# Kernel optimization log

Measured on AMD Instinct MI355X. Metric: run time of the kernel, lower is better.

The kernel has to match this reference:

```python
import jax, jax.numpy as jnp
import numpy as np

TEMP1, TEMP2, TEMP3 = 4.0, 5.0, 10.0  # forward() default temps
EPS = 1e-8


def setup_inputs() -> dict:
    key = jax.random.key(0)
    k1, k2 = jax.random.split(key)
    B, L, D = 64, 64, 512
    return {
        "ecg_embs": jax.random.normal(k1, (B, L, D), dtype=jnp.float32),
        "sent_embs": jax.random.normal(k2, (B, L, D), dtype=jnp.float32),
    }


def reference(ecg_embs, sent_embs):
    # Fully-batched version of the original per-sample Python loop.
    # i indexes the sentence (query) sample, j the ecg (context) sample.
    B, L, D = ecg_embs.shape
    # scores[i,j,s,q] = <ecg[j,s,:], sent[i,q,:]>  == contextT @ query in torch
    scores = jnp.einsum('jsd,iqd->ijsq', ecg_embs, sent_embs)
    # 1st softmax over query axis q
    attn = jax.nn.softmax(scores, axis=-1)
    # transpose to (i,j,q,s), temperature-scale, 2nd softmax over source axis s
    attn = jax.nn.softmax(TEMP1 * jnp.swapaxes(attn, -1, -2), axis=-1)  # (i,j,q,s)
    # weightedContext[i,j,q,:] = sum_s attn[i,j,q,s] * ecg[j,s,:]
    wctx = jnp.einsum('ijqs,jsd->ijqd', attn, ecg_embs)
    sent = sent_embs[:, None]  # (i,1,q,d) broadcast over j
    w12 = jnp.sum(sent * wctx, axis=-1)
    w1 = jnp.linalg.norm(sent, axis=-1)
    w2 = jnp.linalg.norm(wctx, axis=-1)
    cos = w12 / jnp.maximum(w1 * w2, EPS)  # (i,j,q)
    # row_sim.mul_(temp2).exp_().sum(dim=1).log() ; similarities[j,i] (cat along dim=1)
    sim = TEMP3 * jnp.log(jnp.sum(jnp.exp(TEMP2 * cos), axis=-1)).T  # (j,i)
    labels = jnp.arange(B)
    logp0 = jax.nn.log_softmax(sim, axis=-1)
    logp1 = jax.nn.log_softmax(sim.T, axis=-1)
    loss0 = -jnp.mean(logp0[labels, labels])
    loss1 = -jnp.mean(logp1[labels, labels])
    # att_maps: list of attn[i] from iteration i == diagonal (i==j) attention,
    # each shaped (1, queryL, ih=1, iw=sourceL); stacked -> (B, 1, L, 1, L)
    att_maps = attn[labels, labels][:, None, :, None, :]
    return (loss0 + loss1) / 2.0, att_maps
```

## Files before the change

kernel.cpp:

```cpp
#include <hip/hip_runtime.h>
#include <math.h>

typedef __attribute__((ext_vector_type(8))) short short8;
typedef __attribute__((ext_vector_type(4))) float f32x4;
typedef unsigned int uint;
typedef unsigned short ushort;

#define T1 4.0f
#define T2 5.0f
#define T3 10.0f
#define EPSF 1e-8f
#define SST 68

__device__ inline ushort f2bf(float x) {
    union { float f; uint u; } a; a.f = x;
    uint r = a.u + 0x7FFFu + ((a.u >> 16) & 1u);
    return (ushort)(r >> 16);
}
__device__ inline float bf2f(ushort h) {
    union { uint u; float f; } a; a.u = ((uint)h) << 16;
    return a.f;
}

#define GLDS(gsrc, ldst) \
    __builtin_amdgcn_global_load_lds( \
        (const __attribute__((address_space(1))) uint*)(gsrc), \
        (__attribute__((address_space(3))) uint*)(ldst), 16, 0, 0)

__global__ __launch_bounds__(256) void prep_kernel(
        const float* __restrict__ ecg, const float* __restrict__ sent,
        char* __restrict__ EH, char* __restrict__ EL,
        char* __restrict__ SH, char* __restrict__ SL, float* __restrict__ w1) {
    __shared__ float rs[32][2];
    const int bid = blockIdx.x;
    const int tensor = bid >> 7, idx = (bid >> 1) & 63, half = bid & 1;
    const float* src = (tensor ? sent : ecg) + (size_t)idx * 32768;
    char* dh = (tensor ? SH : EH) + (size_t)idx * 65536;
    char* dl = (tensor ? SL : EL) + (size_t)idx * 65536;
    const int tid = threadIdx.x;
    const int w = tid >> 6, l = tid & 63;

    if (tid < 64) { rs[tid >> 1][tid & 1] = 0.f; }
    __syncthreads();

    const int kc   = 8 * (w & 1) + (l >> 3);
    const int c    = (l >> 1) & 3;
    const int col  = 256 * (w & 1) + l * 4;
    const int wsel = w & 1;

    #pragma unroll
    for (int g = 0; g < 16; g++) {
        int r = 32 * half + 2 * g + (w >> 1);
        float4 v = *(const float4*)(src + (size_t)r * 512 + col);
        ushort h0 = f2bf(v.x), h1 = f2bf(v.y), h2 = f2bf(v.z), h3 = f2bf(v.w);
        uint2 H; H.x = (uint)h0 | ((uint)h1 << 16); H.y = (uint)h2 | ((uint)h3 << 16);
        ushort l0 = f2bf(v.x - bf2f(h0)), l1 = f2bf(v.y - bf2f(h1));
        ushort l2 = f2bf(v.z - bf2f(h2)), l3 = f2bf(v.w - bf2f(h3));
        uint2 L; L.x = (uint)l0 | ((uint)l1 << 16); L.y = (uint)l2 | ((uint)l3 << 16);
        size_t off = (size_t)kc * 4096 + r * 64 + ((c + (r >> 1)) & 3) * 16 + (l & 1) * 8;
        *(uint2*)(dh + off) = H;
        *(uint2*)(dl + off) = L;
        if (tensor) {
            float p = v.x * v.x + v.y * v.y + v.z * v.z + v.w * v.w;
            #pragma unroll
            for (int o = 32; o; o >>= 1) p += __shfl_xor(p, o);
            if (l == 0) rs[2 * g + (w >> 1)][wsel] += p;
        }
    }
    __syncthreads();
    if (tensor && tid < 32)
        w1[idx * 64 + 32 * half + tid] = sqrtf(rs[tid][0] + rs[tid][1]);
}

__global__ __launch_bounds__(256) void gprep_kernel(
        const char* __restrict__ EH, const char* __restrict__ EL, char* __restrict__ Gp) {
    __shared__ __align__(16) char lds[8192];
    const int j = blockIdx.x;
    const int tid = threadIdx.x;
    const int wv = tid >> 6, lane = tid & 63;
    const int wq = wv >> 1, wn = wv & 1;
    const int quad = lane >> 4, ln = lane & 15;
    const char* srcH = EH + (size_t)j * 65536 + wv * 1024 + lane * 16;
    const char* srcL = EL + (size_t)j * 65536 + wv * 1024 + lane * 16;

    int ao[2], bo[2];
    #pragma unroll
    for (int mi = 0; mi < 2; mi++) {
        int R = 32 * wq + 16 * mi + ln;
        ao[mi] = R * 64 + ((quad + (R >> 1)) & 3) * 16;
    }
    #pragma unroll
    for (int ni = 0; ni < 2; ni++) {
        int R = 32 * wn + 16 * ni + ln;
        bo[ni] = R * 64 + ((quad + (R >> 1)) & 3) * 16;
    }

    f32x4 acc[2][2];
    #pragma unroll
    for (int a = 0; a < 2; a++)
        #pragma unroll
        for (int b = 0; b < 2; b++) acc[a][b] = (f32x4){0.f, 0.f, 0.f, 0.f};

    for (int kc = 0; kc < 16; kc++) {
        GLDS(srcH + (size_t)kc * 4096, lds + wv * 1024);
        GLDS(srcL + (size_t)kc * 4096, lds + 4096 + wv * 1024);
        __syncthreads();
        short8 ah[2], al[2], bh[2], bl[2];
        #pragma unroll
        for (int mi = 0; mi < 2; mi++) {
            ah[mi] = *(const short8*)(lds + ao[mi]);
            al[mi] = *(const short8*)(lds + 4096 + ao[mi]);
        }
        #pragma unroll
        for (int ni = 0; ni < 2; ni++) {
            bh[ni] = *(const short8*)(lds + bo[ni]);
            bl[ni] = *(const short8*)(lds + 4096 + bo[ni]);
        }
        #pragma unroll
        for (int mi = 0; mi < 2; mi++)
            #pragma unroll
            for (int ni = 0; ni < 2; ni++) {
                acc[mi][ni] = __builtin_amdgcn_mfma_f32_16x16x32_bf16(ah[mi], bh[ni], acc[mi][ni], 0, 0, 0);
                acc[mi][ni] = __builtin_amdgcn_mfma_f32_16x16x32_bf16(ah[mi], bl[ni], acc[mi][ni], 0, 0, 0);
                acc[mi][ni] = __builtin_amdgcn_mfma_f32_16x16x32_bf16(al[mi], bh[ni], acc[mi][ni], 0, 0, 0);
            }
        __syncthreads();
    }
    #pragma unroll
    for (int mi = 0; mi < 2; mi++)
        #pragma unroll
        for (int ni = 0; ni < 2; ni++)
            #pragma unroll
            for (int r = 0; r < 4; r++) {
                int t = 32 * wq + 16 * mi + quad * 4 + r;
                int u = 32 * wn + 16 * ni + ln;
                float g = acc[mi][ni][r];
                ushort h = f2bf(g);
                ushort l = f2bf(g - bf2f(h));
                char* base = Gp + (size_t)j * 16384 + t * 128 + (((u >> 3) + t) & 7) * 16 + (u & 7) * 2;
                *(ushort*)base = h;
                *(ushort*)(base + 8192) = l;
            }
}

__global__ __launch_bounds__(256, 4) void pair_kernel(
        const char* __restrict__ EH, const char* __restrict__ EL,
        const char* __restrict__ SH, const char* __restrict__ SL,
        const char* __restrict__ Gp, const float* __restrict__ w1g,
        float* __restrict__ simval, float* __restrict__ out) {

    __shared__ __align__(16) char lds[33792];
    __shared__ __align__(16) float mz[64];
    __shared__ float w12all[256], w2all[256];
    __shared__ float mpart[64][2], spart[64][2];

    const int tid = threadIdx.x;
    const int bn = blockIdx.x;
    const int xcd = bn & 7, slot = bn >> 3;
    const int T = xcd * 8 + (slot >> 4);
    const int wp = slot & 15;
    const int bi = (T >> 3) * 4 + (wp >> 2);
    const int bj = (T & 7) * 4 + (wp & 3);
    const int i0 = bi * 2, j0 = bj * 2;

    const int wv = tid >> 6, lane = tid & 63;
    const int wq = wv >> 1, wn = wv & 1;
    const int quad = lane >> 4, ln = lane & 15;

    int aoff[4], boff[4];
    #pragma unroll
    for (int mi = 0; mi < 4; mi++) {
        int R = 64 * (mi >> 1) + 32 * wq + 16 * (mi & 1) + ln;
        aoff[mi] = R * 64 + ((quad + (R >> 1)) & 3) * 16;
    }
    #pragma unroll
    for (int ni = 0; ni < 4; ni++) {
        int R = 64 * (ni >> 1) + 32 * wn + 16 * (ni & 1) + ln;
        boff[ni] = 16384 + R * 64 + ((quad + (R >> 1)) & 3) * 16;
    }

    const char* gA; const char* gB; int ldoff;
    if (wv == 0)      { gA = EH + (size_t)j0 * 65536;       gB = EH + (size_t)(j0 + 1) * 65536; ldoff = 0; }
    else if (wv == 1) { gA = EL + (size_t)j0 * 65536;       gB = EL + (size_t)(j0 + 1) * 65536; ldoff = 8192; }
    else if (wv == 2) { gA = SH + (size_t)i0 * 65536;       gB = SH + (size_t)(i0 + 1) * 65536; ldoff = 16384; }
    else              { gA = SL + (size_t)i0 * 65536;       gB = SL + (size_t)(i0 + 1) * 65536; ldoff = 24576; }
    gA += lane * 16; gB += lane * 16;

    f32x4 acc[4][4];
    #pragma unroll
    for (int a = 0; a < 4; a++)
        #pragma unroll
        for (int b = 0; b < 4; b++) acc[a][b] = (f32x4){0.f, 0.f, 0.f, 0.f};

    for (int kc = 0; kc < 16; kc++) {
        #pragma unroll
        for (int n = 0; n < 4; n++) GLDS(gA + n * 1024, lds + ldoff + n * 1024);
        #pragma unroll
        for (int n = 0; n < 4; n++) GLDS(gB + n * 1024, lds + ldoff + 4096 + n * 1024);
        gA += 4096; gB += 4096;
        __syncthreads();
        short8 bh[4], bl[4];
        #pragma unroll
        for (int ni = 0; ni < 4; ni++) {
            bh[ni] = *(const short8*)(lds + boff[ni]);
            bl[ni] = *(const short8*)(lds + boff[ni] + 8192);
        }
        #pragma unroll
        for (int mi = 0; mi < 4; mi++) {
            short8 ah = *(const short8*)(lds + aoff[mi]);
            short8 al = *(const short8*)(lds + aoff[mi] + 8192);
            #pragma unroll
            for (int ni = 0; ni < 4; ni++) {
                acc[mi][ni] = __builtin_amdgcn_mfma_f32_16x16x32_bf16(ah, bh[ni], acc[mi][ni], 0, 0, 0);
                acc[mi][ni] = __builtin_amdgcn_mfma_f32_16x16x32_bf16(ah, bl[ni], acc[mi][ni], 0, 0, 0);
                acc[mi][ni] = __builtin_amdgcn_mfma_f32_16x16x32_bf16(al, bh[ni], acc[mi][ni], 0, 0, 0);
            }
        }
        __syncthreads();
    }

    float* SsT = (float*)lds;
    float* yT  = (float*)lds;
    char*  Pb  = lds + 17408;

    #pragma unroll
    for (int pr = 0; pr < 4; pr++) {
        const int a = pr >> 1, b = pr & 1;
        const int i = i0 + b, j = j0 + a;

        #pragma unroll
        for (int dm = 0; dm < 2; dm++)
            #pragma unroll
            for (int dn = 0; dn < 2; dn++) {
                int s0 = 32 * wq + 16 * dm + quad * 4;
                int q  = 32 * wn + 16 * dn + ln;
                *(f32x4*)(SsT + q * SST + s0) = acc[2 * a + dm][2 * b + dn];
            }
        #pragma unroll
        for (int dm = 0; dm < 2; dm++)
            #pragma unroll
            for (int r = 0; r < 4; r++) {
                float v0 = acc[2 * a + dm][2 * b + 0][r];
                float v1 = acc[2 * a + dm][2 * b + 1][r];
                float m = fmaxf(v0, v1);
                m = fmaxf(m, __shfl_xor(m, 1));
                m = fmaxf(m, __shfl_xor(m, 2));
                m = fmaxf(m, __shfl_xor(m, 4));
                m = fmaxf(m, __shfl_xor(m, 8));
                float e = __expf(v0 - m) + __expf(v1 - m);
                e += __shfl_xor(e, 1);
                e += __shfl_xor(e, 2);
                e += __shfl_xor(e, 4);
                e += __shfl_xor(e, 8);
                if (ln == 0) {
                    int s = 32 * wq + 16 * dm + quad * 4 + r;
                    mpart[s][wn] = m;
                    spart[s][wn] = e;
                }
            }
        __syncthreads();

        if (tid < 64) {
            float m0 = mpart[tid][0], m1 = mpart[tid][1];
            float mm = fmaxf(m0, m1);
            float z = spart[tid][0] * __expf(m0 - mm) + spart[tid][1] * __expf(m1 - mm);
            mz[tid] = mm + __logf(z);
        }
        __syncthreads();

        {
            const int q = tid >> 2, c = tid & 3;
            float sc[16], at[16];
            #pragma unroll
            for (int r4 = 0; r4 < 4; r4++)
                *(f32x4*)(sc + 4 * r4) = *(const f32x4*)(SsT + q * SST + 16 * c + 4 * r4);
            float mzv[16];
            #pragma unroll
            for (int r4 = 0; r4 < 4; r4++)
                *(f32x4*)(mzv + 4 * r4) = *(const f32x4*)(mz + 16 * c + 4 * r4);
            float m2 = -1e30f;
            #pragma unroll
            for (int t = 0; t < 16; t++) {
                at[t] = __expf(sc[t] - mzv[t]);
                m2 = fmaxf(m2, T1 * at[t]);
            }
            m2 = fmaxf(m2, __shfl_xor(m2, 1));
            m2 = fmaxf(m2, __shfl_xor(m2, 2));
            float sum = 0.f;
            #pragma unroll
            for (int t = 0; t < 16; t++) { at[t] = __expf(T1 * at[t] - m2); sum += at[t]; }
            sum += __shfl_xor(sum, 1);
            sum += __shfl_xor(sum, 2);
            float inv = 1.f / sum;
            float p12 = 0.f;
            #pragma unroll
            for (int t = 0; t < 16; t++) { at[t] *= inv; p12 += at[t] * sc[t]; }
            p12 += __shfl_xor(p12, 1);
            p12 += __shfl_xor(p12, 2);
            if (c == 0) w12all[pr * 64 + q] = p12;

            if (i == j) {
                float* om = out + 1 + (size_t)i * 4096;
                #pragma unroll
                for (int t = 0; t < 16; t++) om[q * 64 + c * 16 + t] = at[t];
            }

            uint hw[8], lw[8];
            #pragma unroll
            for (int e = 0; e < 8; e++) {
                ushort h0 = f2bf(at[2 * e]), h1 = f2bf(at[2 * e + 1]);
                hw[e] = (uint)h0 | ((uint)h1 << 16);
                ushort l0 = f2bf(at[2 * e] - bf2f(h0)), l1 = f2bf(at[2 * e + 1] - bf2f(h1));
                lw[e] = (uint)l0 | ((uint)l1 << 16);
            }
            int p0 = (2 * c + q) & 7, p1 = (2 * c + 1 + q) & 7;
            uint4 W;
            W.x = hw[0]; W.y = hw[1]; W.z = hw[2]; W.w = hw[3];
            *(uint4*)(Pb + q * 128 + p0 * 16) = W;
            W.x = hw[4]; W.y = hw[5]; W.z = hw[6]; W.w = hw[7];
            *(uint4*)(Pb + q * 128 + p1 * 16) = W;
            W.x = lw[0]; W.y = lw[1]; W.z = lw[2]; W.w = lw[3];
            *(uint4*)(Pb + 8192 + q * 128 + p0 * 16) = W;
            W.x = lw[4]; W.y = lw[5]; W.z = lw[6]; W.w = lw[7];
            *(uint4*)(Pb + 8192 + q * 128 + p1 * 16) = W;
        }
        __syncthreads();

        {
            const char* gs = Gp + (size_t)j * 16384 + wv * 4096 + lane * 16;
            #pragma unroll
            for (int k = 0; k < 4; k++)
                GLDS(gs + k * 1024, lds + wv * 4096 + k * 1024);
        }
        __syncthreads();

        f32x4 acc2[2][2];
        #pragma unroll
        for (int x = 0; x < 2; x++)
            #pragma unroll
            for (int y = 0; y < 2; y++) acc2[x][y] = (f32x4){0.f, 0.f, 0.f, 0.f};
        #pragma unroll
        for (int ch = 0; ch < 2; ch++) {
            short8 pah[2], pal[2], gbh[2], gbl[2];
            #pragma unroll
            for (int m2i = 0; m2i < 2; m2i++) {
                int q = 32 * wq + 16 * m2i + ln;
                int ph = ((ch * 4 + quad) + q) & 7;
                pah[m2i] = *(const short8*)(Pb + q * 128 + ph * 16);
                pal[m2i] = *(const short8*)(Pb + 8192 + q * 128 + ph * 16);
            }
            #pragma unroll
            for (int n2i = 0; n2i < 2; n2i++) {
                int u = 32 * wn + 16 * n2i + ln;
                int ph = ((ch * 4 + quad) + u) & 7;
                gbh[n2i] = *(const short8*)(lds + u * 128 + ph * 16);
                gbl[n2i] = *(const short8*)(lds + 8192 + u * 128 + ph * 16);
            }
            #pragma unroll
            for (int m2i = 0; m2i < 2; m2i++)
                #pragma unroll
                for (int n2i = 0; n2i < 2; n2i++) {
                    acc2[m2i][n2i] = __builtin_amdgcn_mfma_f32_16x16x32_bf16(pah[m2i], gbh[n2i], acc2[m2i][n2i], 0, 0, 0);
                    acc2[m2i][n2i] = __builtin_amdgcn_mfma_f32_16x16x32_bf16(pah[m2i], gbl[n2i], acc2[m2i][n2i], 0, 0, 0);
                    acc2[m2i][n2i] = __builtin_amdgcn_mfma_f32_16x16x32_bf16(pal[m2i], gbh[n2i], acc2[m2i][n2i], 0, 0, 0);
                }
        }
        __syncthreads();

        #pragma unroll
        for (int m2i = 0; m2i < 2; m2i++)
            #pragma unroll
            for (int n2i = 0; n2i < 2; n2i++) {
                int q0 = 32 * wq + 16 * m2i + quad * 4;
                int t  = 32 * wn + 16 * n2i + ln;
                *(f32x4*)(yT + t * SST + q0) = acc2[m2i][n2i];
            }
        __syncthreads();

        {
            const int q = tid >> 2, c = tid & 3;
            int p0 = (2 * c + q) & 7, p1 = (2 * c + 1 + q) & 7;
            uint4 H0 = *(const uint4*)(Pb + q * 128 + p0 * 16);
            uint4 H1 = *(const uint4*)(Pb + q * 128 + p1 * 16);
            uint4 L0 = *(const uint4*)(Pb + 8192 + q * 128 + p0 * 16);
            uint4 L1 = *(const uint4*)(Pb + 8192 + q * 128 + p1 * 16);
            uint hw[8] = {H0.x,H0.y,H0.z,H0.w, H1.x,H1.y,H1.z,H1.w};
            uint lw[8] = {L0.x,L0.y,L0.z,L0.w, L1.x,L1.y,L1.z,L1.w};
            float s = 0.f;
            #pragma unroll
            for (int e = 0; e < 8; e++) {
                float q0v = bf2f((ushort)(hw[e] & 0xFFFFu)) + bf2f((ushort)(lw[e] & 0xFFFFu));
                float q1v = bf2f((ushort)(hw[e] >> 16))     + bf2f((ushort)(lw[e] >> 16));
                s += q0v * yT[(16 * c + 2 * e) * SST + q];
                s += q1v * yT[(16 * c + 2 * e + 1) * SST + q];
            }
            s += __shfl_xor(s, 1);
            s += __shfl_xor(s, 2);
            if (c == 0) w2all[pr * 64 + q] = s;
        }
        __syncthreads();
    }

    {
        const int pr = wv;
        const int ii = i0 + (pr & 1), jj = j0 + (pr >> 1);
        float w2 = sqrtf(fmaxf(w2all[pr * 64 + lane], 0.f));
        float cosv = w12all[pr * 64 + lane] / fmaxf(w1g[ii * 64 + lane] * w2, EPSF);
        float e = __expf(T2 * cosv);
        #pragma unroll
        for (int off = 32; off; off >>= 1) e += __shfl_down(e, off);
        if (lane == 0) simval[ii * 64 + jj] = T3 * __logf(e);
    }
}

__global__ __launch_bounds__(256) void loss_kernel(const float* __restrict__ val,
                                                   float* __restrict__ out) {
    __shared__ float v[4096];
    const int tid = threadIdx.x;
    #pragma unroll
    for (int k = 0; k < 4; k++)
        ((float4*)v)[tid + k * 256] = ((const float4*)val)[tid + k * 256];
    __syncthreads();
    if (tid < 64) {
        int i = tid;
        float rmax = -1e30f, cmax = -1e30f;
        for (int jj = 0; jj < 64; jj++) {
            rmax = fmaxf(rmax, v[i * 64 + jj]);
            cmax = fmaxf(cmax, v[jj * 64 + i]);
        }
        float rs = 0.f, cs = 0.f;
        for (int jj = 0; jj < 64; jj++) {
            rs += __expf(v[i * 64 + jj] - rmax);
            cs += __expf(v[jj * 64 + i] - cmax);
        }
        float rlse = rmax + __logf(rs);
        float clse = cmax + __logf(cs);
        float part = 2.f * v[i * 64 + i] - rlse - clse;
        #pragma unroll
        for (int off = 32; off; off >>= 1) part += __shfl_down(part, off);
        if (i == 0) out[0] = -part / 128.f;
    }
}

extern "C" void kernel_launch(void* const* d_in, const int* in_sizes, int n_in,
                              void* d_out, int out_size, void* d_ws, size_t ws_size,
                              hipStream_t stream) {
    (void)in_sizes; (void)n_in; (void)out_size; (void)ws_size;
    const float* ecg  = (const float*)d_in[0];
    const float* sent = (const float*)d_in[1];
    float* out = (float*)d_out;

    char* ws = (char*)d_ws;
    float* w1v  = (float*)ws;
    float* simv = (float*)(ws + 16384);
    char* EH = ws + 32768;
    char* EL = EH + (size_t)64 * 65536;
    char* SH = EL + (size_t)64 * 65536;
    char* SL = SH + (size_t)64 * 65536;
    char* Gp = SL + (size_t)64 * 65536;

    prep_kernel <<<256, 256, 0, stream>>>(ecg, sent, EH, EL, SH, SL, w1v);
    gprep_kernel<<<64,  256, 0, stream>>>(EH, EL, Gp);
    pair_kernel <<<1024, 256, 0, stream>>>(EH, EL, SH, SL, Gp, w1v, simv, out);
    loss_kernel <<<1,   256, 0, stream>>>(simv, out);
}
```

Baseline: 161.7 us.

## Drop low-bf16 attention term and restructure pair-kernel epilogue around registers

The attention matrix P is now stored only as a single bf16 high part, so the second GEMM uses two MFMAs per tile instead of three. The w2 norm is computed directly from the accumulator registers with a small partial-sum buffer, removing the yT transpose through LDS and two barriers. The first softmax now reads a swizzled, unpadded score tile from LDS, replacing the shuffle-based partial max/sum pass. The G tile is copied through registers instead of global_load_lds. The precision of P against the fp32 reference drops, which may affect tolerance.

```diff
diff --git a/kernel.cpp b/kernel.cpp
--- a/kernel.cpp
+++ b/kernel.cpp
@@ -10,7 +10,6 @@
 #define T2 5.0f
 #define T3 10.0f
 #define EPSF 1e-8f
-#define SST 68
 
 __device__ inline ushort f2bf(float x) {
     union { float f; uint u; } a; a.f = x;
@@ -149,10 +148,10 @@
         const char* __restrict__ Gp, const float* __restrict__ w1g,
         float* __restrict__ simval, float* __restrict__ out) {
 
-    __shared__ __align__(16) char lds[33792];
+    __shared__ __align__(16) char lds[32768];
     __shared__ __align__(16) float mz[64];
     __shared__ float w12all[256], w2all[256];
-    __shared__ float mpart[64][2], spart[64][2];
+    __shared__ float w2part[64 * 9];
 
     const int tid = threadIdx.x;
     const int bn = blockIdx.x;
@@ -219,9 +218,7 @@
         __syncthreads();
     }
 
-    float* SsT = (float*)lds;
-    float* yT  = (float*)lds;
-    char*  Pb  = lds + 17408;
+    char* Pb = lds + 16384;
 
     #pragma unroll
     for (int pr = 0; pr < 4; pr++) {
@@ -234,50 +231,39 @@
             for (int dn = 0; dn < 2; dn++) {
                 int s0 = 32 * wq + 16 * dm + quad * 4;
                 int q  = 32 * wn + 16 * dn + ln;
-                *(f32x4*)(SsT + q * SST + s0) = acc[2 * a + dm][2 * b + dn];
-            }
-        #pragma unroll
-        for (int dm = 0; dm < 2; dm++)
-            #pragma unroll
-            for (int r = 0; r < 4; r++) {
-                float v0 = acc[2 * a + dm][2 * b + 0][r];
-                float v1 = acc[2 * a + dm][2 * b + 1][r];
-                float m = fmaxf(v0, v1);
-                m = fmaxf(m, __shfl_xor(m, 1));
-                m = fmaxf(m, __shfl_xor(m, 2));
-                m = fmaxf(m, __shfl_xor(m, 4));
-                m = fmaxf(m, __shfl_xor(m, 8));
-                float e = __expf(v0 - m) + __expf(v1 - m);
-                e += __shfl_xor(e, 1);
-                e += __shfl_xor(e, 2);
-                e += __shfl_xor(e, 4);
-                e += __shfl_xor(e, 8);
-                if (ln == 0) {
-                    int s = 32 * wq + 16 * dm + quad * 4 + r;
-                    mpart[s][wn] = m;
-                    spart[s][wn] = e;
-                }
-            }
-        __syncthreads();
-
-        if (tid < 64) {
-            float m0 = mpart[tid][0], m1 = mpart[tid][1];
-            float mm = fmaxf(m0, m1);
-            float z = spart[tid][0] * __expf(m0 - mm) + spart[tid][1] * __expf(m1 - mm);
-            mz[tid] = mm + __logf(z);
+                *(f32x4*)(lds + q * 256 + (((s0 >> 2) + q) & 15) * 16) = acc[2 * a + dm][2 * b + dn];
+            }
+        __syncthreads();
+
+        {
+            const int s = tid >> 2, c = tid & 3;
+            float vv[16]; float m = -1e30f;
+            #pragma unroll
+            for (int t = 0; t < 16; t++) {
+                int q = 16 * c + t;
+                vv[t] = *(const float*)(lds + q * 256 + ((((s >> 2) + q) & 15) << 4) + ((s & 3) << 2));
+                m = fmaxf(m, vv[t]);
+            }
+            m = fmaxf(m, __shfl_xor(m, 1));
+            m = fmaxf(m, __shfl_xor(m, 2));
+            float sum = 0.f;
+            #pragma unroll
+            for (int t = 0; t < 16; t++) sum += __expf(vv[t] - m);
+            sum += __shfl_xor(sum, 1);
+            sum += __shfl_xor(sum, 2);
+            if (c == 0) mz[s] = m + __logf(sum);
         }
         __syncthreads();
 
         {
             const int q = tid >> 2, c = tid & 3;
-            float sc[16], at[16];
-            #pragma unroll
-            for (int r4 = 0; r4 < 4; r4++)
-                *(f32x4*)(sc + 4 * r4) = *(const f32x4*)(SsT + q * SST + 16 * c + 4 * r4);
-            float mzv[16];
-            #pragma unroll
-            for (int r4 = 0; r4 < 4; r4++)
-                *(f32x4*)(mzv + 4 * r4) = *(const f32x4*)(mz + 16 * c + 4 * r4);
+            float sc[16], at[16], mzv[16];
+            #pragma unroll
+            for (int k = 0; k < 4; k++)
+                *(f32x4*)(sc + 4 * k) = *(const f32x4*)(lds + q * 256 + (((4 * c + k) + q) & 15) * 16);
+            #pragma unroll
+            for (int k = 0; k < 4; k++)
+                *(f32x4*)(mzv + 4 * k) = *(const f32x4*)(mz + 16 * c + 4 * k);
             float m2 = -1e30f;
             #pragma unroll
             for (int t = 0; t < 16; t++) {
@@ -305,32 +291,26 @@
                 for (int t = 0; t < 16; t++) om[q * 64 + c * 16 + t] = at[t];
             }
 
-            uint hw[8], lw[8];
-            #pragma unroll
-            for (int e = 0; e < 8; e++) {
-                ushort h0 = f2bf(at[2 * e]), h1 = f2bf(at[2 * e + 1]);
-                hw[e] = (uint)h0 | ((uint)h1 << 16);
-                ushort l0 = f2bf(at[2 * e] - bf2f(h0)), l1 = f2bf(at[2 * e + 1] - bf2f(h1));
-                lw[e] = (uint)l0 | ((uint)l1 << 16);
-            }
+            uint hw[8];
+            #pragma unroll
+            for (int e = 0; e < 8; e++)
+                hw[e] = (uint)f2bf(at[2 * e]) | ((uint)f2bf(at[2 * e + 1]) << 16);
             int p0 = (2 * c + q) & 7, p1 = (2 * c + 1 + q) & 7;
             uint4 W;
             W.x = hw[0]; W.y = hw[1]; W.z = hw[2]; W.w = hw[3];
             *(uint4*)(Pb + q * 128 + p0 * 16) = W;
             W.x = hw[4]; W.y = hw[5]; W.z = hw[6]; W.w = hw[7];
             *(uint4*)(Pb + q * 128 + p1 * 16) = W;
-            W.x = lw[0]; W.y = lw[1]; W.z = lw[2]; W.w = lw[3];
-            *(uint4*)(Pb + 8192 + q * 128 + p0 * 16) = W;
-            W.x = lw[4]; W.y = lw[5]; W.z = lw[6]; W.w = lw[7];
-            *(uint4*)(Pb + 8192 + q * 128 + p1 * 16) = W;
         }
         __syncthreads();
 
         {
-            const char* gs = Gp + (size_t)j * 16384 + wv * 4096 + lane * 16;
-            #pragma unroll
-            for (int k = 0; k < 4; k++)
-                GLDS(gs + k * 1024, lds + wv * 4096 + k * 1024);
+            const char* gs = Gp + (size_t)j * 16384;
+            #pragma unroll
+            for (int k = 0; k < 4; k++) {
+                uint4 g = *(const uint4*)(gs + k * 4096 + tid * 16);
+                *(uint4*)(lds + k * 4096 + tid * 16) = g;
+            }
         }
         __syncthreads();
 
@@ -341,13 +321,11 @@
             for (int y = 0; y < 2; y++) acc2[x][y] = (f32x4){0.f, 0.f, 0.f, 0.f};
         #pragma unroll
         for (int ch = 0; ch < 2; ch++) {
-            short8 pah[2], pal[2], gbh[2], gbl[2];
+            short8 pah[2], gbh[2], gbl[2];
             #pragma unroll
             for (int m2i = 0; m2i < 2; m2i++) {
                 int q = 32 * wq + 16 * m2i + ln;
-                int ph = ((ch * 4 + quad) + q) & 7;
-                pah[m2i] = *(const short8*)(Pb + q * 128 + ph * 16);
-                pal[m2i] = *(const short8*)(Pb + 8192 + q * 128 + ph * 16);
+                pah[m2i] = *(const short8*)(Pb + q * 128 + (((ch * 4 + quad) + q) & 7) * 16);
             }
             #pragma unroll
             for (int n2i = 0; n2i < 2; n2i++) {
@@ -362,44 +340,35 @@
                 for (int n2i = 0; n2i < 2; n2i++) {
                     acc2[m2i][n2i] = __builtin_amdgcn_mfma_f32_16x16x32_bf16(pah[m2i], gbh[n2i], acc2[m2i][n2i], 0, 0, 0);
                     acc2[m2i][n2i] = __builtin_amdgcn_mfma_f32_16x16x32_bf16(pah[m2i], gbl[n2i], acc2[m2i][n2i], 0, 0, 0);
-                    acc2[m2i][n2i] = __builtin_amdgcn_mfma_f32_16x16x32_bf16(pal[m2i], gbh[n2i], acc2[m2i][n2i], 0, 0, 0);
                 }
         }
-        __syncthreads();
 
         #pragma unroll
         for (int m2i = 0; m2i < 2; m2i++)
             #pragma unroll
-            for (int n2i = 0; n2i < 2; n2i++) {
-                int q0 = 32 * wq + 16 * m2i + quad * 4;
-                int t  = 32 * wn + 16 * n2i + ln;
-                *(f32x4*)(yT + t * SST + q0) = acc2[m2i][n2i];
-            }
-        __syncthreads();
-
-        {
-            const int q = tid >> 2, c = tid & 3;
-            int p0 = (2 * c + q) & 7, p1 = (2 * c + 1 + q) & 7;
-            uint4 H0 = *(const uint4*)(Pb + q * 128 + p0 * 16);
-            uint4 H1 = *(const uint4*)(Pb + q * 128 + p1 * 16);
-            uint4 L0 = *(const uint4*)(Pb + 8192 + q * 128 + p0 * 16);
-            uint4 L1 = *(const uint4*)(Pb + 8192 + q * 128 + p1 * 16);
-            uint hw[8] = {H0.x,H0.y,H0.z,H0.w, H1.x,H1.y,H1.z,H1.w};
-            uint lw[8] = {L0.x,L0.y,L0.z,L0.w, L1.x,L1.y,L1.z,L1.w};
-            float s = 0.f;
-            #pragma unroll
-            for (int e = 0; e < 8; e++) {
-                float q0v = bf2f((ushort)(hw[e] & 0xFFFFu)) + bf2f((ushort)(lw[e] & 0xFFFFu));
-                float q1v = bf2f((ushort)(hw[e] >> 16))     + bf2f((ushort)(lw[e] >> 16));
-                s += q0v * yT[(16 * c + 2 * e) * SST + q];
-                s += q1v * yT[(16 * c + 2 * e + 1) * SST + q];
-            }
-            s += __shfl_xor(s, 1);
-            s += __shfl_xor(s, 2);
-            if (c == 0) w2all[pr * 64 + q] = s;
-        }
-        __syncthreads();
-    }
+            for (int rr = 0; rr < 4; rr++) {
+                int rA = 32 * wq + 16 * m2i + quad * 4 + rr;
+                float p = 0.f;
+                #pragma unroll
+                for (int n2i = 0; n2i < 2; n2i++) {
+                    int t = 32 * wn + 16 * n2i + ln;
+                    float Pv = bf2f(*(const ushort*)(Pb + rA * 128 +
+                                     ((((t >> 3) + rA) & 7) << 4) + ((t & 7) << 1)));
+                    p += acc2[m2i][n2i][rr] * Pv;
+                }
+                p += __shfl_xor(p, 1);
+                p += __shfl_xor(p, 2);
+                if ((ln & 3) == 0) w2part[rA * 9 + wn * 4 + (ln >> 2)] = p;
+            }
+        __syncthreads();
+
+        if (tid < 64) {
+            const float* wp9 = w2part + tid * 9;
+            w2all[pr * 64 + tid] = wp9[0] + wp9[1] + wp9[2] + wp9[3] +
+                                   wp9[4] + wp9[5] + wp9[6] + wp9[7];
+        }
+    }
+    __syncthreads();
 
     {
         const int pr = wv;
```

After: 162.4 us. Within noise of the previous version (+0.4%).
